# Optimization experiments

Hardware: AMD Instinct MI355X
Metric: run time of the kernel (lower is better)

Reference implementation:

```python
import jax, jax.numpy as jnp
import numpy as np

NB, H, C, HID, EMB = 4, 12, 1024, 768, 512
E, M, L, SPAN = 22, 4, 16, 32
TD, INTER = 20, 256
NN = E + E * M + L
NREL, NLAYERS = 3, 4

def _build_adj():
    # static relational adjacency: r0 entity<->its mentions, r1 mention<->co-entity mention, r2 mention<->link
    A = np.zeros((NREL, NN, NN), np.float32)
    for e in range(E):
        for m in range(M):
            mi = E + e * M + m
            A[0, e, mi] = A[0, mi, e] = 1.0
            for m2 in range(M):
                if m2 != m:
                    A[1, mi, E + e * M + m2] = 1.0
            li = E + E * M + ((e * M + m) % L)
            A[2, mi, li] = A[2, li, mi] = 1.0
    A = A / (A.sum(-1, keepdims=True) + 1e-5)
    return jnp.asarray(A)

_ADJ = _build_adj()
_TYPES = np.concatenate([np.zeros(E, np.int32), np.ones(E * M, np.int32), np.full(L, 2, np.int32)])

def _forward(sequence_output, attention, W_trans, b_trans, type_embed,
             rgcn_Wrel0, rgcn_Wself0, rgcn_Wrel, rgcn_Wself,
             fs_w1, fs_b1, fs_g1, fs_be1, fs_w2, fs_b2, fs_g2, fs_be2,
             fc_w1, fc_b1, fc_g1, fc_be1, fc_w2, fc_b2, fc_g2, fc_be2,
             cr_w1, cr_b1, cr_w2, cr_b2, cr_w3, cr_b3,
             mention_idx, link_start):
    n = sequence_output.shape[0]
    b = jnp.arange(n)[:, None, None]
    seq = sequence_output @ W_trans + b_trans            # [n,C,EMB] extractor_trans
    attq = attention.transpose(0, 2, 1, 3)               # [n,C,H,C] query-major
    # --- make_graph: mention / entity nodes (gather + logsumexp pooling) ---
    m_rep = seq[b, mention_idx]                          # [n,E,M,EMB]
    m_att = attq[b, mention_idx]                         # [n,E,M,H,C]
    e_rep = jax.nn.logsumexp(m_rep, axis=2)              # [n,E,EMB]
    e_att = m_att.mean(axis=2)                           # [n,E,H,C]
    # --- link nodes: attention-weighted span pooling ---
    idx = link_start[:, :, None] + jnp.arange(SPAN)      # [n,L,SPAN]
    span = seq[b, idx]                                   # [n,L,SPAN,EMB]
    att_rows = attq[b, idx]                              # [n,L,SPAN,H,C]
    col_idx = jnp.broadcast_to(idx[:, :, None, None, :], (n, L, SPAN, H, SPAN))
    block = jnp.take_along_axis(att_rows, col_idx, axis=4).mean(axis=3)  # [n,L,SPAN,SPAN]
    link_rep = jnp.einsum('nlst,nltd->nld', block, span) / SPAN          # [n,L,EMB]
    # --- node matrix + type embedding ---
    nodes = jnp.concatenate([e_rep, m_rep.reshape(n, E * M, EMB), link_rep], axis=1)
    tfeat = jnp.broadcast_to(type_embed[_TYPES][None], (n, NN, TD))
    h = jnp.concatenate([nodes, tfeat], axis=-1)         # [n,NN,EMB+TD]
    # --- RGCN ---
    def rgcn_layer(hh, Wrel, Wself):
        msg = jnp.einsum('rij,njd,rdo->nio', _ADJ, hh, Wrel)
        return jax.nn.relu(msg + hh @ Wself)
    h = rgcn_layer(h, rgcn_Wrel0, rgcn_Wself0)
    for l in range(NLAYERS - 1):
        h = rgcn_layer(h, rgcn_Wrel[l], rgcn_Wself[l])
    # --- relation_map: structure + attention-weighted context ---
    entity_stru = h[:, :E]                               # [n,E,EMB]
    ea = e_att.mean(axis=2)                              # [n,E,C]
    ea = ea / (ea.sum(-1, keepdims=True) + 1e-5)
    e_ctx = jnp.einsum('nec,ncd->ned', ea, seq)          # [n,E,EMB]
    ec = entity_stru + e_ctx
    fmap = (ec[:, :, None, :] * ec[:, None, :, :]).transpose(0, 3, 1, 2)  # [n,EMB,E,E]
    # --- SE fusion (fusion_s / fusion_c, BN in eval form) ---
    conv1x1 = lambda x, w, bb: jnp.einsum('nchw,oc->nohw', x, w) + bb[None, :, None, None]
    bn = lambda x, g, be: x * g[None, :, None, None] + be[None, :, None, None]
    s = bn(conv1x1(jax.nn.relu(bn(conv1x1(fmap, fs_w1, fs_b1), fs_g1, fs_be1)), fs_w2, fs_b2), fs_g2, fs_be2)
    pooled = fmap.mean(axis=(2, 3), keepdims=True)
    cb = bn(conv1x1(jax.nn.relu(bn(conv1x1(pooled, fc_w1, fc_b1), fc_g1, fc_be1)), fc_w2, fc_b2), fc_g2, fc_be2)
    fused = fmap * jax.nn.sigmoid(s + cb)
    # --- conv_reason 5x5 blocks ---
    dn = ('NCHW', 'OIHW', 'NCHW')
    conv = lambda x, w, bb: jax.lax.conv_general_dilated(x, w, (1, 1), 'SAME', dimension_numbers=dn) + bb[None, :, None, None]
    r = jax.nn.relu(conv(fused, cr_w1, cr_b1))
    r = jax.nn.relu(conv(r, cr_w2, cr_b2))
    return jax.nn.relu(conv(r, cr_w3, cr_b3))            # [n,EMB,E,E]

def setup_inputs():
    key = jax.random.key(0)
    ks = jax.random.split(key, 24)
    p = lambda k, sh: jax.random.normal(k, sh, jnp.float32) * 0.02
    z = lambda sh: jnp.zeros(sh, jnp.float32)
    o = lambda sh: jnp.ones(sh, jnp.float32)
    return {
        'sequence_output': jax.random.normal(ks[0], (NB, C, HID), jnp.float32),
        'attention': jax.random.uniform(ks[1], (NB, H, C, C), jnp.float32),
        'W_trans': p(ks[2], (HID, EMB)), 'b_trans': z((EMB,)),
        'type_embed': p(ks[3], (3, TD)),
        'rgcn_Wrel0': p(ks[4], (NREL, EMB + TD, EMB)), 'rgcn_Wself0': p(ks[5], (EMB + TD, EMB)),
        'rgcn_Wrel': p(ks[6], (NLAYERS - 1, NREL, EMB, EMB)), 'rgcn_Wself': p(ks[7], (NLAYERS - 1, EMB, EMB)),
        'fs_w1': p(ks[8], (INTER, EMB)), 'fs_b1': z((INTER,)), 'fs_g1': o((INTER,)), 'fs_be1': z((INTER,)),
        'fs_w2': p(ks[9], (EMB, INTER)), 'fs_b2': z((EMB,)), 'fs_g2': o((EMB,)), 'fs_be2': z((EMB,)),
        'fc_w1': p(ks[10], (INTER, EMB)), 'fc_b1': z((INTER,)), 'fc_g1': o((INTER,)), 'fc_be1': z((INTER,)),
        'fc_w2': p(ks[11], (EMB, INTER)), 'fc_b2': z((EMB,)), 'fc_g2': o((EMB,)), 'fc_be2': z((EMB,)),
        'cr_w1': p(ks[12], (INTER, EMB, 5, 5)), 'cr_b1': z((INTER,)),
        'cr_w2': p(ks[13], (INTER, INTER, 5, 5)), 'cr_b2': z((INTER,)),
        'cr_w3': p(ks[14], (EMB, INTER, 5, 5)), 'cr_b3': z((EMB,)),
        'mention_idx': jax.random.randint(ks[15], (NB, E, M), 0, C),
        'link_start': jnp.sort(jax.random.randint(ks[16], (NB, L), 0, C - SPAN), axis=-1),
    }

def reference(sequence_output, attention, W_trans, b_trans, type_embed,
              rgcn_Wrel0, rgcn_Wself0, rgcn_Wrel, rgcn_Wself,
              fs_w1, fs_b1, fs_g1, fs_be1, fs_w2, fs_b2, fs_g2, fs_be2,
              fc_w1, fc_b1, fc_g1, fc_be1, fc_w2, fc_b2, fc_g2, fc_be2,
              cr_w1, cr_b1, cr_w2, cr_b2, cr_w3, cr_b3,
              mention_idx, link_start):
    return _forward(sequence_output, attention, W_trans, b_trans, type_embed,
                    rgcn_Wrel0, rgcn_Wself0, rgcn_Wrel, rgcn_Wself,
                    fs_w1, fs_b1, fs_g1, fs_be1, fs_w2, fs_b2, fs_g2, fs_be2,
                    fc_w1, fc_b1, fc_g1, fc_be1, fc_w2, fc_b2, fc_g2, fc_be2,
                    cr_w1, cr_b1, cr_w2, cr_b2, cr_w3, cr_b3,
                    mention_idx, link_start)
```

## Files before the change

kernel.cpp:

```cpp
#include <hip/hip_runtime.h>
#include <hip/hip_bf16.h>
#include <stdint.h>

typedef long long ll;
typedef float f32x4 __attribute__((ext_vector_type(4)));
typedef __bf16 bf16x8 __attribute__((ext_vector_type(8)));
typedef __bf16 bf16x4 __attribute__((ext_vector_type(4)));

__global__ void k_prep(const float* __restrict__ cr_w1, const float* __restrict__ cr_w2,
                       const float* __restrict__ cr_w3, __bf16* __restrict__ Wt1,
                       __bf16* __restrict__ Wt2, __bf16* __restrict__ Wt3,
                       const float* __restrict__ W_trans, __bf16* __restrict__ wth,
                       __bf16* __restrict__ wtl,
                       const float* __restrict__ Wrel0, const float* __restrict__ Wself0,
                       __bf16* __restrict__ wc0h, __bf16* __restrict__ wc0l,
                       const float* __restrict__ Wrel, const float* __restrict__ Wself,
                       __bf16* __restrict__ wc13h, __bf16* __restrict__ wc13l)
{
  __shared__ float t[32][33];
  int b = blockIdx.x; int tid = threadIdx.x;
  if (b < 1024){
    const float* w; __bf16* dst; int C, o;
    if (b < 256){ w=cr_w1; dst=Wt1; C=512; o=b; }
    else if (b < 512){ w=cr_w2; dst=Wt2; C=256; o=b-256; }
    else { w=cr_w3; dst=Wt3; C=256; o=b-512; }
    for (int c=tid; c<C; c+=256){
      const float* src = w + ((size_t)o*C + c)*25;
      float v[25];
      #pragma unroll
      for (int q=0;q<25;q++) v[q] = src[q];
      #pragma unroll
      for (int q=0;q<25;q++) dst[((size_t)o*25 + q)*C + c] = (__bf16)v[q];
    }
  } else if (b < 2560){
    ll idx = (ll)(b-1024)*256 + tid;
    int r = (int)(idx % 768); int c = (int)(idx / 768);
    float x = W_trans[(ll)r*512 + c];
    __bf16 h = (__bf16)x;
    wth[idx] = h; wtl[idx] = (__bf16)(x - (float)h);
  } else {
    int Din, Kpad, bx, by;
    const float* wr; const float* ws2; __bf16* hb; __bf16* lb;
    if (b < 3648){
      int b2 = b-2560; bx = b2 % 68; by = b2/68; Din=532; Kpad=2176;
      wr = Wrel0; ws2 = Wself0; hb = wc0h; lb = wc0l;
    } else {
      int b3 = b-3648; int l = b3/1024; int r2 = b3%1024; bx = r2%64; by = r2/64;
      Din=512; Kpad=2048;
      wr = Wrel + (ll)l*3*512*512; ws2 = Wself + (ll)l*512*512;
      hb = wc13h + (ll)l*512*2048; lb = wc13l + (ll)l*512*2048;
    }
    int k0 = bx*32, o0 = by*32;
    int tx = tid&31, ty = tid>>5;
    for (int j=ty; j<32; j+=8){
      int k = k0 + j; float v = 0.f;
      if (k < 3*Din) v = wr[(ll)k*512 + o0+tx];
      else if (k < 4*Din) v = ws2[(ll)(k-3*Din)*512 + o0+tx];
      t[j][tx] = v;
    }
    __syncthreads();
    for (int j=ty; j<32; j+=8){
      float x = t[tx][j];
      __bf16 h = (__bf16)x;
      hb[(ll)(o0+j)*Kpad + k0+tx] = h;
      lb[(ll)(o0+j)*Kpad + k0+tx] = (__bf16)(x - (float)h);
    }
  }
}

template<int SPLIT, int MODE, int BN>
__global__ __launch_bounds__(512) void gemm_mfma(
    const float* __restrict__ A,
    const __bf16* __restrict__ Bhi, const __bf16* __restrict__ Blo,
    float* __restrict__ Cf, __bf16* __restrict__ Cb,
    int M, int N, int K, ll sA, ll sB, ll sC,
    const float* __restrict__ biasN, const float* __restrict__ biasM,
    const float* __restrict__ gM, const float* __restrict__ beM,
    const __bf16* __restrict__ Fm, const float* __restrict__ CBV)
{
  constexpr int NF = BN/32;
  constexpr int SL = (4096 + BN*64) * (SPLIT?2:1);
  constexpr int REDB = 256*2*NF*16;
  constexpr int LDSB = (2*SL > REDB) ? 2*SL : REDB;
  __shared__ char lds[LDSB];

  int b = blockIdx.z;
  A += sA*b; Bhi += sB*b; if (SPLIT) Blo += sB*b;

  const int tid = threadIdx.x;
  const int slice = tid>>8;
  const int tl = tid & 255;
  const int w4 = (tid>>6)&3;
  const int grp = tid>>8;
  const int l15 = tid&15, lg=(tid&63)>>4, lg16=lg*16;
  const int wave_m0=(w4>>1)*32, wave_n0=(w4&1)*(BN/2);
  const int m0 = blockIdx.y*64, n0 = blockIdx.x*BN;

  char* sA_H = lds + slice*SL;
  char* sB_H = sA_H + 4096;
  char* sA_L = sB_H + BN*64;
  char* sB_L = sA_L + 4096;

  const int sa_row=tl>>2, sa_c8=tl&3;
  const int sa_byte = sa_row*64 + ((sa_c8*16) ^ (((sa_row>>1)&3)<<4));
  const int gmA = m0 + sa_row;

  int baseA[2], baseB[NF];
  #pragma unroll
  for (int mf=0; mf<2; ++mf){
    int r = wave_m0 + mf*16 + l15;
    baseA[mf] = r*64 + (lg16 ^ (((r>>1)&3)<<4));
  }
  #pragma unroll
  for (int nf=0; nf<NF; ++nf){
    int r = wave_n0 + nf*16 + l15;
    baseB[nf] = r*64 + (lg16 ^ (((r>>1)&3)<<4));
  }

  f32x4 acc[2][NF] = {};

  for (int k0=0; k0<K; k0+=64){
    int kk = k0 + slice*32;
    __syncthreads();
    {
      float f[8] = {0,0,0,0,0,0,0,0};
      if (gmA < M){
        float4 p0 = *reinterpret_cast<const float4*>(A + (ll)gmA*K + kk + sa_c8*8);
        float4 p1 = *reinterpret_cast<const float4*>(A + (ll)gmA*K + kk + sa_c8*8 + 4);
        f[0]=p0.x; f[1]=p0.y; f[2]=p0.z; f[3]=p0.w;
        f[4]=p1.x; f[5]=p1.y; f[6]=p1.z; f[7]=p1.w;
      }
      bf16x8 h, l;
      #pragma unroll
      for (int j=0;j<8;j++){
        h[j] = (__bf16)f[j];
        if (SPLIT) l[j] = (__bf16)(f[j] - (float)h[j]);
      }
      *reinterpret_cast<bf16x8*>(sA_H + sa_byte) = h;
      if (SPLIT) *reinterpret_cast<bf16x8*>(sA_L + sa_byte) = l;
    }
    #pragma unroll
    for (int i=0;i<BN/64;i++){
      int idx = tl + i*256;
      int row = idx>>2, c8 = idx&3;
      int gn = n0 + row;
      int byte = row*64 + ((c8*16) ^ (((row>>1)&3)<<4));
      bf16x8 v = {};
      if (gn < N) v = *reinterpret_cast<const bf16x8*>(Bhi + (ll)gn*K + kk + c8*8);
      *reinterpret_cast<bf16x8*>(sB_H + byte) = v;
      if (SPLIT){
        bf16x8 vl = {};
        if (gn < N) vl = *reinterpret_cast<const bf16x8*>(Blo + (ll)gn*K + kk + c8*8);
        *reinterpret_cast<bf16x8*>(sB_L + byte) = vl;
      }
    }
    __syncthreads();
    bf16x8 aH[2], bH[NF];
    #pragma unroll
    for (int mf=0; mf<2; ++mf) aH[mf] = *reinterpret_cast<const bf16x8*>(sA_H + baseA[mf]);
    #pragma unroll
    for (int nf=0; nf<NF; ++nf) bH[nf] = *reinterpret_cast<const bf16x8*>(sB_H + baseB[nf]);
    if (SPLIT){
      bf16x8 aL[2], bL[NF];
      #pragma unroll
      for (int mf=0; mf<2; ++mf) aL[mf] = *reinterpret_cast<const bf16x8*>(sA_L + baseA[mf]);
      #pragma unroll
      for (int nf=0; nf<NF; ++nf) bL[nf] = *reinterpret_cast<const bf16x8*>(sB_L + baseB[nf]);
      #pragma unroll
      for (int mf=0; mf<2; ++mf)
        #pragma unroll
        for (int nf=0; nf<NF; ++nf){
          acc[mf][nf] = __builtin_amdgcn_mfma_f32_16x16x32_bf16(aH[mf], bH[nf], acc[mf][nf], 0,0,0);
          acc[mf][nf] = __builtin_amdgcn_mfma_f32_16x16x32_bf16(aH[mf], bL[nf], acc[mf][nf], 0,0,0);
          acc[mf][nf] = __builtin_amdgcn_mfma_f32_16x16x32_bf16(aL[mf], bH[nf], acc[mf][nf], 0,0,0);
        }
    } else {
      #pragma unroll
      for (int mf=0; mf<2; ++mf)
        #pragma unroll
        for (int nf=0; nf<NF; ++nf)
          acc[mf][nf] = __builtin_amdgcn_mfma_f32_16x16x32_bf16(aH[mf], bH[nf], acc[mf][nf], 0,0,0);
    }
  }

  __syncthreads();
  if (grp==1){
    char* rp = lds + (ll)(tid-256)*(2*NF*16);
    #pragma unroll
    for (int mf=0; mf<2; ++mf)
      #pragma unroll
      for (int nf=0; nf<NF; ++nf)
        *reinterpret_cast<f32x4*>(rp + (mf*NF+nf)*16) = acc[mf][nf];
  }
  __syncthreads();
  if (grp!=0) return;
  {
    char* rp = lds + (ll)tid*(2*NF*16);
    #pragma unroll
    for (int mf=0; mf<2; ++mf)
      #pragma unroll
      for (int nf=0; nf<NF; ++nf)
        acc[mf][nf] += *reinterpret_cast<f32x4*>(rp + (mf*NF+nf)*16);
  }

  if (MODE==0 || MODE==1){
    float* C = Cf + sC*b;
    #pragma unroll
    for (int mf=0; mf<2; ++mf){
      int gmb = m0 + wave_m0 + mf*16 + lg*4;
      #pragma unroll
      for (int nf=0; nf<NF; ++nf){
        int gn = n0 + wave_n0 + nf*16 + l15;
        if (gn >= N) continue;
        float bn_ = (MODE==0 && biasN) ? biasN[gn] : 0.f;
        f32x4 a = acc[mf][nf];
        #pragma unroll
        for (int r=0;r<4;r++){
          int gm = gmb + r;
          if (gm < M){
            float v = a[r] + bn_;
            if (MODE==1) v = fmaxf(v, 0.f);
            C[(ll)gm*N + gn] = v;
          }
        }
      }
    }
  } else if (MODE==2){
    __bf16* C = Cb + sC*b;
    #pragma unroll
    for (int mf=0; mf<2; ++mf){
      int gmb = m0 + wave_m0 + mf*16 + lg*4;
      float b0=biasM[gmb], b1=biasM[gmb+1], b2=biasM[gmb+2], b3=biasM[gmb+3];
      float g0=gM[gmb], g1=gM[gmb+1], g2=gM[gmb+2], g3=gM[gmb+3];
      float e0=beM[gmb], e1=beM[gmb+1], e2=beM[gmb+2], e3=beM[gmb+3];
      #pragma unroll
      for (int nf=0; nf<NF; ++nf){
        int gn = n0 + wave_n0 + nf*16 + l15;
        if (gn >= N) continue;
        f32x4 a = acc[mf][nf];
        union { bf16x4 v; uint2 u; } pk;
        pk.v[0] = (__bf16)fmaxf((a[0]+b0)*g0+e0, 0.f);
        pk.v[1] = (__bf16)fmaxf((a[1]+b1)*g1+e1, 0.f);
        pk.v[2] = (__bf16)fmaxf((a[2]+b2)*g2+e2, 0.f);
        pk.v[3] = (__bf16)fmaxf((a[3]+b3)*g3+e3, 0.f);
        *reinterpret_cast<uint2*>(C + (ll)gn*M + gmb) = pk.u;
      }
    }
  } else {
    __bf16* C = Cb + sC*b;
    const __bf16* fm = Fm + (ll)b*484*512;
    const float* cb = CBV + (ll)b*512;
    #pragma unroll
    for (int mf=0; mf<2; ++mf){
      int gmb = m0 + wave_m0 + mf*16 + lg*4;
      float b0=biasM[gmb], b1=biasM[gmb+1], b2=biasM[gmb+2], b3=biasM[gmb+3];
      float g0=gM[gmb], g1=gM[gmb+1], g2=gM[gmb+2], g3=gM[gmb+3];
      float e0=beM[gmb], e1=beM[gmb+1], e2=beM[gmb+2], e3=beM[gmb+3];
      float c0=cb[gmb], c1=cb[gmb+1], c2=cb[gmb+2], c3=cb[gmb+3];
      #pragma unroll
      for (int nf=0; nf<NF; ++nf){
        int gn = n0 + wave_n0 + nf*16 + l15;
        if (gn >= N) continue;
        f32x4 a = acc[mf][nf];
        bf16x4 fmv = *reinterpret_cast<const bf16x4*>(fm + (ll)gn*512 + gmb);
        float s0 = (a[0]+b0)*g0+e0 + c0;
        float s1 = (a[1]+b1)*g1+e1 + c1;
        float s2 = (a[2]+b2)*g2+e2 + c2;
        float s3 = (a[3]+b3)*g3+e3 + c3;
        union { bf16x4 v; uint2 u; } pk;
        pk.v[0] = (__bf16)((float)fmv[0] / (1.f + expf(-s0)));
        pk.v[1] = (__bf16)((float)fmv[1] / (1.f + expf(-s1)));
        pk.v[2] = (__bf16)((float)fmv[2] / (1.f + expf(-s2)));
        pk.v[3] = (__bf16)((float)fmv[3] / (1.f + expf(-s3)));
        int py = gn/22, px = gn%22;
        int e = (py+2)*32 + px + 2;
        *reinterpret_cast<uint2*>(C + (ll)e*512 + gmb) = pk.u;
      }
    }
  }
}

template<int CIN, int OCHT, bool FINAL>
__global__ __launch_bounds__(256) void conv5_mfma(
    const __bf16* __restrict__ Xg, const __bf16* __restrict__ Wt,
    const float* __restrict__ bias, __bf16* __restrict__ Xout,
    float* __restrict__ outF)
{
  __shared__ bf16x8 Xs8[272*32/8];
  __shared__ bf16x8 Ws8[5*64*32/8];
  char* xs = (char*)Xs8;
  char* wsm = (char*)Ws8;

  const int tid = threadIdx.x;
  const int l = tid & 63;
  const int l15 = l & 15, lg = l >> 4, lg16 = (l>>4)*16;
  const int w = tid >> 6;
  const int wave_o0 = (w>>1)*32;
  const int wave_p0 = (w&1)*64;
  const int b = blockIdx.z;
  const int p0 = blockIdx.x*128;
  const int o0 = blockIdx.y*64;

  int orow0 = wave_o0 + l15;
  int orow1 = wave_o0 + 16 + l15;
  int baseA0 = orow0*64 + (lg16 ^ (((orow0>>1)&3)<<4));
  int baseA1 = orow1*64 + (lg16 ^ (((orow1>>1)&3)<<4));
  int pl[4];
  #pragma unroll
  for (int pf=0; pf<4; ++pf) pl[pf] = wave_p0 + pf*16 + l15;

  f32x4 acc[2][4] = {};

  const int NCB = CIN/32;
  for (int cblk=0; cblk<NCB; ++cblk){
    __syncthreads();
    #pragma unroll
    for (int i=0;i<5;i++){
      int idx = tid + i*256;
      if (idx < 1088){
        int e = idx>>2, c8 = idx&3;
        const __bf16* g = Xg + ((size_t)(b*928 + p0 + e))*CIN + cblk*32 + c8*8;
        bf16x8 v = *reinterpret_cast<const bf16x8*>(g);
        int byte = e*64 + ((c8*16) ^ (((e>>1)&3)<<4));
        *reinterpret_cast<bf16x8*>(xs + byte) = v;
      }
    }
    for (int g5=0; g5<5; ++g5){
      if (g5>0) __syncthreads();
      #pragma unroll
      for (int i=0;i<5;i++){
        int idx = tid + i*256;
        int tapL = idx>>8, r = idx&255;
        int o = r>>2, c8 = r&3;
        const __bf16* g = Wt + ((size_t)(o0+o)*25 + (g5*5+tapL))*CIN + cblk*32 + c8*8;
        bf16x8 v = *reinterpret_cast<const bf16x8*>(g);
        int byte = tapL*4096 + o*64 + ((c8*16) ^ (((o>>1)&3)<<4));
        *reinterpret_cast<bf16x8*>(wsm + byte) = v;
      }
      __syncthreads();
      #pragma unroll
      for (int tapL=0; tapL<5; ++tapL){
        bf16x8 a0 = *reinterpret_cast<const bf16x8*>(wsm + tapL*4096 + baseA0);
        bf16x8 a1 = *reinterpret_cast<const bf16x8*>(wsm + tapL*4096 + baseA1);
        int koff = g5*32 + tapL;
        #pragma unroll
        for (int pf=0; pf<4; ++pf){
          int e = pl[pf] + koff;
          bf16x8 bv = *reinterpret_cast<const bf16x8*>(xs + e*64 + (lg16 ^ (((e>>1)&3)<<4)));
          acc[0][pf] = __builtin_amdgcn_mfma_f32_16x16x32_bf16(a0, bv, acc[0][pf], 0,0,0);
          acc[1][pf] = __builtin_amdgcn_mfma_f32_16x16x32_bf16(a1, bv, acc[1][pf], 0,0,0);
        }
      }
    }
  }

  #pragma unroll
  for (int of=0; of<2; ++of){
    int og = o0 + wave_o0 + of*16 + lg*4;
    float b0 = bias[og], b1 = bias[og+1], b2 = bias[og+2], b3 = bias[og+3];
    #pragma unroll
    for (int pf=0; pf<4; ++pf){
      int p = p0 + pl[pf];
      int py = p>>5, px = p&31;
      if (py>=22 || px>=22) continue;
      f32x4 a = acc[of][pf];
      float v0 = fmaxf(a[0]+b0, 0.f), v1 = fmaxf(a[1]+b1, 0.f);
      float v2 = fmaxf(a[2]+b2, 0.f), v3 = fmaxf(a[3]+b3, 0.f);
      if (FINAL){
        size_t base = ((size_t)b*OCHT + og)*484 + py*22 + px;
        outF[base] = v0; outF[base+484] = v1; outF[base+968] = v2; outF[base+1452] = v3;
      } else {
        union { bf16x4 v; uint2 u; } pk;
        pk.v[0] = (__bf16)v0; pk.v[1] = (__bf16)v1; pk.v[2] = (__bf16)v2; pk.v[3] = (__bf16)v3;
        int e = p + 66;
        *reinterpret_cast<uint2*>(Xout + ((size_t)(b*928 + e))*OCHT + og) = pk.u;
      }
    }
  }
}

__global__ void k_gather(const float* __restrict__ seq, const float* __restrict__ att,
                         const int* __restrict__ midx, const int* __restrict__ ls_,
                         const float* __restrict__ te, float* __restrict__ h0,
                         float* __restrict__ ea, __bf16* __restrict__ sqTh,
                         __bf16* __restrict__ sqTl)
{
  __shared__ float part[32][8];
  __shared__ float wv[32];
  __shared__ float vals[1024];
  __shared__ float red[256];
  __shared__ float tt2[32][33];
  int b = blockIdx.x; int t = threadIdx.x;
  if (b < 88){
    int n = b/22, e = b%22;
    int rows[4];
    #pragma unroll
    for (int m=0;m<4;m++) rows[m] = midx[(n*22+e)*4+m];
    for (int d=t; d<512; d+=256){
      float v[4]; float mx = -1e30f;
      #pragma unroll
      for (int m=0;m<4;m++){
        v[m] = seq[((ll)n*1024+rows[m])*512 + d];
        h0[((ll)n*126+22+e*4+m)*532 + d] = v[m];
        mx = fmaxf(mx, v[m]);
      }
      float s = 0.f;
      #pragma unroll
      for (int m=0;m<4;m++) s += expf(v[m]-mx);
      h0[((ll)n*126+e)*532 + d] = mx + logf(s);
    }
  } else if (b < 152){
    int bb = b-88;
    int n = bb/16, l = bb%16;
    int ls = ls_[n*16+l];
    int tt = t>>3, lane = t&7;
    float acc = 0.f;
    for (int i=lane; i<384; i+=8){
      int h = i>>5, s = i&31;
      acc += att[((ll)(n*12+h)*1024 + ls+s)*1024 + (ls+tt)];
    }
    part[tt][lane] = acc; __syncthreads();
    if (lane==0){
      float s2=0.f;
      #pragma unroll
      for (int q=0;q<8;q++) s2 += part[tt][q];
      wv[tt] = s2*(1.f/12.f);
    }
    __syncthreads();
    for (int d=t; d<512; d+=256){
      float a2 = 0.f;
      for (int tk=0;tk<32;tk++) a2 += wv[tk]*seq[((ll)n*1024+ls+tk)*512 + d];
      h0[((ll)n*126+110+l)*532 + d] = a2*(1.f/32.f);
    }
  } else if (b < 192){
    int idx = (b-152)*256 + t;
    if (idx < 4*126*20){
      int q = idx%20; int i = (idx/20)%126; int n = idx/(20*126);
      int ty = (i<22)?0:((i<110)?1:2);
      h0[((ll)n*126+i)*532 + 512 + q] = te[ty*20+q];
    }
  } else if (b < 280){
    int bb = b-192;
    int n = bb/22, e = bb%22;
    int rows[4];
    #pragma unroll
    for (int m=0;m<4;m++) rows[m] = midx[(n*22+e)*4+m];
    float local = 0.f;
    for (int c=t; c<1024; c+=256){
      float acc = 0.f;
      #pragma unroll
      for (int m=0;m<4;m++){
        const float* base = att + ((ll)n*12*1024 + rows[m])*1024 + c;
        #pragma unroll
        for (int h=0;h<12;h++) acc += base[(ll)h*1048576];
      }
      acc *= (1.f/48.f);
      vals[c] = acc; local += acc;
    }
    red[t] = local; __syncthreads();
    for (int s=128;s>0;s>>=1){ if (t<s) red[t]+=red[t+s]; __syncthreads(); }
    float denom = red[0] + 1e-5f;
    for (int c=t; c<1024; c+=256) ea[((ll)bb)*1024 + c] = vals[c]/denom;
  } else {
    int b2 = b-280;
    int n = b2>>9; int rem = b2&511;
    int r0 = (rem&31)*32, c0 = (rem>>5)*32;
    int tx = t&31, ty = t>>5;
    for (int j=ty; j<32; j+=8)
      tt2[j][tx] = seq[((ll)n*1024 + r0+j)*512 + c0+tx];
    __syncthreads();
    for (int j=ty; j<32; j+=8){
      float x = tt2[tx][j];
      __bf16 h = (__bf16)x;
      ll o = ((ll)n*512 + c0+j)*1024 + r0+tx;
      sqTh[o] = h; sqTl[o] = (__bf16)(x - (float)h);
    }
  }
}

__global__ void k_buildX_s(const float* __restrict__ h, float* __restrict__ X,
                           int Din, int ldX){
  int n = blockIdx.x/126, i = blockIdx.x%126;
  const float* hb = h + (ll)n*126*Din;
  ll rowoff = (ll)(n*126+i)*ldX;
  const float inv1 = 1.f/(1.f+1e-5f), inv3 = 1.f/(3.f+1e-5f), inv4 = 1.f/(4.f+1e-5f);
  for (int d=threadIdx.x; d<Din; d+=256){
    float m0v=0.f, m1v=0.f, m2v=0.f;
    if (i < 22){
      int base = 22 + i*4;
      float s = hb[(ll)(base+0)*Din+d] + hb[(ll)(base+1)*Din+d]
              + hb[(ll)(base+2)*Din+d] + hb[(ll)(base+3)*Din+d];
      m0v = s * inv4;
    } else if (i < 110){
      int em = i-22, e = em>>2, base = 22+(e<<2);
      m0v = hb[(ll)e*Din+d] * inv1;
      float s1 = 0.f;
      #pragma unroll
      for (int m2=0;m2<4;m2++) if (base+m2 != i) s1 += hb[(ll)(base+m2)*Din+d];
      m1v = s1 * inv3;
      m2v = hb[(ll)(110+(em&15))*Din+d] * inv1;
    } else {
      int li0 = i-110;
      int cnt = (li0<8)?6:5;
      float s = 0.f;
      for (int t2=0;t2<cnt;t2++) s += hb[(ll)(22+li0+16*t2)*Din+d];
      m2v = s / ((float)cnt + 1e-5f);
    }
    float hh = hb[(ll)i*Din+d];
    X[rowoff + 0*Din + d] = m0v;
    X[rowoff + 1*Din + d] = m1v;
    X[rowoff + 2*Din + d] = m2v;
    X[rowoff + 3*Din + d] = hh;
  }
  for (int k=4*Din+threadIdx.x; k<ldX; k+=256) X[rowoff + k] = 0.f;
}

__global__ void k_fmap2(const float* __restrict__ hfin, const float* __restrict__ ectx,
                        __bf16* __restrict__ fmapT,
                        const float* __restrict__ w1, const float* __restrict__ b1,
                        const float* __restrict__ g1, const float* __restrict__ be1,
                        const float* __restrict__ w2, const float* __restrict__ b2,
                        const float* __restrict__ g2, const float* __restrict__ be2,
                        float* __restrict__ cb){
  __shared__ float ps[512], t1[256];
  int b = blockIdx.x; int t = threadIdx.x;
  if (b < 3872){
    int idx = b*256 + t;
    int ch = idx & 511; int p = (idx>>9) % 484; int n = idx/(484*512);
    int i = p/22, j = p%22;
    float vi = hfin[((ll)n*126+i)*512 + ch] + ectx[((ll)n*22+i)*512 + ch];
    float vj = hfin[((ll)n*126+j)*512 + ch] + ectx[((ll)n*22+j)*512 + ch];
    fmapT[idx] = (__bf16)(vi*vj);
  } else {
    int n = b-3872;
    for (int c=t; c<512; c+=256){
      float s = 0.f;
      for (int i=0;i<22;i++)
        s += hfin[((ll)n*126+i)*512 + c] + ectx[((ll)n*22+i)*512 + c];
      ps[c] = s*s*(1.f/484.f);
    }
    __syncthreads();
    {
      float acc = 0.f;
      for (int c=0;c<512;c++) acc += w1[t*512+c]*ps[c];
      float v = g1[t]*(acc+b1[t]) + be1[t];
      t1[t] = fmaxf(v, 0.f);
    }
    __syncthreads();
    for (int o=t; o<512; o+=256){
      float acc = 0.f;
      for (int c=0;c<256;c++) acc += w2[o*256+c]*t1[c];
      cb[n*512+o] = g2[o]*(acc+b2[o]) + be2[o];
    }
  }
}

extern "C" void kernel_launch(void* const* d_in, const int* in_sizes, int n_in,
                              void* d_out, int out_size, void* d_ws, size_t ws_size,
                              hipStream_t stream)
{
  (void)in_sizes; (void)n_in; (void)out_size; (void)ws_size;
  const float* seqout   = (const float*)d_in[0];
  const float* att      = (const float*)d_in[1];
  const float* W_trans  = (const float*)d_in[2];
  const float* b_trans  = (const float*)d_in[3];
  const float* type_emb = (const float*)d_in[4];
  const float* Wrel0    = (const float*)d_in[5];
  const float* Wself0   = (const float*)d_in[6];
  const float* Wrel     = (const float*)d_in[7];
  const float* Wself    = (const float*)d_in[8];
  const float* fs_w1    = (const float*)d_in[9];
  const float* fs_b1    = (const float*)d_in[10];
  const float* fs_g1    = (const float*)d_in[11];
  const float* fs_be1   = (const float*)d_in[12];
  const float* fs_w2    = (const float*)d_in[13];
  const float* fs_b2    = (const float*)d_in[14];
  const float* fs_g2    = (const float*)d_in[15];
  const float* fs_be2   = (const float*)d_in[16];
  const float* fc_w1    = (const float*)d_in[17];
  const float* fc_b1    = (const float*)d_in[18];
  const float* fc_g1    = (const float*)d_in[19];
  const float* fc_be1   = (const float*)d_in[20];
  const float* fc_w2    = (const float*)d_in[21];
  const float* fc_b2    = (const float*)d_in[22];
  const float* fc_g2    = (const float*)d_in[23];
  const float* fc_be2   = (const float*)d_in[24];
  const float* cr_w1    = (const float*)d_in[25];
  const float* cr_b1    = (const float*)d_in[26];
  const float* cr_w2    = (const float*)d_in[27];
  const float* cr_b2    = (const float*)d_in[28];
  const float* cr_w3    = (const float*)d_in[29];
  const float* cr_b3    = (const float*)d_in[30];
  const int*   midx     = (const int*)d_in[31];
  const int*   lstart   = (const int*)d_in[32];
  float* out            = (float*)d_out;

  char* wsb = (char*)d_ws;
  size_t off = 0;
  auto allocB = [&](size_t nbytes)->char*{ char* p = wsb + off; off += (nbytes + 63) & ~(size_t)63; return p; };
  float* seq   = (float*)allocB((size_t)4096*512*4);
  float* h0    = (float*)allocB((size_t)504*532*4);
  float* ea    = (float*)allocB((size_t)88*1024*4);
  float* ectx  = (float*)allocB((size_t)88*512*4);
  float* X     = (float*)allocB((size_t)504*2176*4);
  float* hA    = (float*)allocB((size_t)504*512*4);
  float* hB    = (float*)allocB((size_t)504*512*4);
  float* cbv   = (float*)allocB(2048*4);
  __bf16* wth  = (__bf16*)allocB((size_t)512*768*2);
  __bf16* wtl  = (__bf16*)allocB((size_t)512*768*2);
  __bf16* sqTh = (__bf16*)allocB((size_t)4*512*1024*2);
  __bf16* sqTl = (__bf16*)allocB((size_t)4*512*1024*2);
  __bf16* wc0h = (__bf16*)allocB((size_t)512*2176*2);
  __bf16* wc0l = (__bf16*)allocB((size_t)512*2176*2);
  __bf16* wc13h= (__bf16*)allocB((size_t)3*512*2048*2);
  __bf16* wc13l= (__bf16*)allocB((size_t)3*512*2048*2);
  __bf16* fmapT= (__bf16*)allocB((size_t)4*484*512*2);
  __bf16* s1bT = (__bf16*)allocB((size_t)4*484*256*2);
  __bf16* Xint1 = (__bf16*)allocB((size_t)4*928*512*2);
  __bf16* Xint2 = (__bf16*)allocB((size_t)4*928*256*2);
  __bf16* Xint3 = (__bf16*)allocB((size_t)4*928*256*2);
  __bf16* Wt1   = (__bf16*)allocB((size_t)256*25*512*2);
  __bf16* Wt2   = (__bf16*)allocB((size_t)256*25*256*2);
  __bf16* Wt3   = (__bf16*)allocB((size_t)512*25*256*2);

  (void)hipMemsetAsync(Xint1, 0, (size_t)(4*928*512 + 4*928*256 + 4*928*256)*2, stream);

  k_prep<<<6720,256,0,stream>>>(cr_w1, cr_w2, cr_w3, Wt1, Wt2, Wt3,
                                W_trans, wth, wtl,
                                Wrel0, Wself0, wc0h, wc0l,
                                Wrel, Wself, wc13h, wc13l);

  gemm_mfma<1,0,128><<<dim3(4,64,1),512,0,stream>>>(seqout, wth, wtl, seq, nullptr,
      4096,512,768, 0,0,0, b_trans,nullptr,nullptr,nullptr, nullptr,nullptr);
  k_gather<<<2328,256,0,stream>>>(seq, att, midx, lstart, type_emb, h0, ea, sqTh, sqTl);
  gemm_mfma<1,0,64><<<dim3(8,1,4),512,0,stream>>>(ea, sqTh, sqTl, ectx, nullptr,
      22,512,1024, (ll)22*1024, (ll)512*1024, (ll)22*512,
      nullptr,nullptr,nullptr,nullptr, nullptr,nullptr);
  k_buildX_s<<<504,256,0,stream>>>(h0, X, 532, 2176);
  gemm_mfma<1,1,64><<<dim3(8,8,1),512,0,stream>>>(X, wc0h, wc0l, hA, nullptr,
      504,512,2176, 0,0,0, nullptr,nullptr,nullptr,nullptr, nullptr,nullptr);
  float* hcur = hA; float* hnxt = hB;
  for (int l=0;l<3;l++){
    k_buildX_s<<<504,256,0,stream>>>(hcur, X, 512, 2048);
    gemm_mfma<1,1,64><<<dim3(8,8,1),512,0,stream>>>(X,
        wc13h + (ll)l*512*2048, wc13l + (ll)l*512*2048, hnxt, nullptr,
        504,512,2048, 0,0,0, nullptr,nullptr,nullptr,nullptr, nullptr,nullptr);
    float* t = hcur; hcur = hnxt; hnxt = t;
  }
  k_fmap2<<<3876,256,0,stream>>>(hcur, ectx, fmapT,
                                 fc_w1, fc_b1, fc_g1, fc_be1,
                                 fc_w2, fc_b2, fc_g2, fc_be2, cbv);
  gemm_mfma<0,2,64><<<dim3(8,4,4),512,0,stream>>>(fs_w1, fmapT, nullptr, nullptr, s1bT,
      256,484,512, 0, (ll)484*512, (ll)484*256,
      nullptr, fs_b1, fs_g1, fs_be1, nullptr,nullptr);
  gemm_mfma<0,4,64><<<dim3(8,8,4),512,0,stream>>>(fs_w2, s1bT, nullptr, nullptr, Xint1,
      512,484,256, 0, (ll)484*256, (ll)928*512,
      nullptr, fs_b2, fs_g2, fs_be2, fmapT, cbv);
  conv5_mfma<512,256,false><<<dim3(6,4,4),256,0,stream>>>(Xint1, Wt1, cr_b1, Xint2, nullptr);
  conv5_mfma<256,256,false><<<dim3(6,4,4),256,0,stream>>>(Xint2, Wt2, cr_b2, Xint3, nullptr);
  conv5_mfma<256,512,true ><<<dim3(6,8,4),256,0,stream>>>(Xint3, Wt3, cr_b3, nullptr, out);
}
```

Baseline: 532.9 us.

## Fuse RGCN message aggregation into GEMM A-load and compute entity context directly

Removes the k_buildX_s kernels by having the RGCN GEMM build its A tile on the fly, aggregating neighbour rows per relation from the static adjacency structure. The self and weight layout is padded per relation block (KD) so each 8-wide chunk maps to a single relation. The entity-context GEMM and the bf16 transpose of seq are replaced by a direct weighted sum inside k_gather. This cuts four launches and the X round trip through memory. In exchange the GEMM A-loads become scalar, gathered and redundant, and the per-block context loop is serial over 1024 rows.

```diff
diff --git a/kernel.cpp b/kernel.cpp
--- a/kernel.cpp
+++ b/kernel.cpp
@@ -39,14 +39,14 @@
     __bf16 h = (__bf16)x;
     wth[idx] = h; wtl[idx] = (__bf16)(x - (float)h);
   } else {
-    int Din, Kpad, bx, by;
+    int Din, Kpad, KD, bx, by;
     const float* wr; const float* ws2; __bf16* hb; __bf16* lb;
     if (b < 3648){
-      int b2 = b-2560; bx = b2 % 68; by = b2/68; Din=532; Kpad=2176;
+      int b2 = b-2560; bx = b2 % 68; by = b2/68; Din=532; Kpad=2176; KD=544;
       wr = Wrel0; ws2 = Wself0; hb = wc0h; lb = wc0l;
     } else {
       int b3 = b-3648; int l = b3/1024; int r2 = b3%1024; bx = r2%64; by = r2/64;
-      Din=512; Kpad=2048;
+      Din=512; Kpad=2048; KD=512;
       wr = Wrel + (ll)l*3*512*512; ws2 = Wself + (ll)l*512*512;
       hb = wc13h + (ll)l*512*2048; lb = wc13l + (ll)l*512*2048;
     }
@@ -54,8 +54,9 @@
     int tx = tid&31, ty = tid>>5;
     for (int j=ty; j<32; j+=8){
       int k = k0 + j; float v = 0.f;
-      if (k < 3*Din) v = wr[(ll)k*512 + o0+tx];
-      else if (k < 4*Din) v = ws2[(ll)(k-3*Din)*512 + o0+tx];
+      int r = k / KD, d = k - r*KD;
+      if (d < Din && r < 4)
+        v = (r<3) ? wr[((ll)(r*Din+d))*512 + o0+tx] : ws2[(ll)d*512 + o0+tx];
       t[j][tx] = v;
     }
     __syncthreads();
@@ -68,7 +69,7 @@
   }
 }
 
-template<int SPLIT, int MODE, int BN>
+template<int SPLIT, int MODE, int BN, int RGCN>
 __global__ __launch_bounds__(512) void gemm_mfma(
     const float* __restrict__ A,
     const __bf16* __restrict__ Bhi, const __bf16* __restrict__ Blo,
@@ -76,7 +77,8 @@
     int M, int N, int K, ll sA, ll sB, ll sC,
     const float* __restrict__ biasN, const float* __restrict__ biasM,
     const float* __restrict__ gM, const float* __restrict__ beM,
-    const __bf16* __restrict__ Fm, const float* __restrict__ CBV)
+    const __bf16* __restrict__ Fm, const float* __restrict__ CBV,
+    int Din, int KD)
 {
   constexpr int NF = BN/32;
   constexpr int SL = (4096 + BN*64) * (SPLIT?2:1);
@@ -105,6 +107,9 @@
   const int sa_byte = sa_row*64 + ((sa_c8*16) ^ (((sa_row>>1)&3)<<4));
   const int gmA = m0 + sa_row;
 
+  int rg_n = 0, rg_i = 0;
+  if (RGCN){ rg_n = gmA/126; rg_i = gmA - rg_n*126; }
+
   int baseA[2], baseB[NF];
   #pragma unroll
   for (int mf=0; mf<2; ++mf){
@@ -124,11 +129,62 @@
     __syncthreads();
     {
       float f[8] = {0,0,0,0,0,0,0,0};
-      if (gmA < M){
-        float4 p0 = *reinterpret_cast<const float4*>(A + (ll)gmA*K + kk + sa_c8*8);
-        float4 p1 = *reinterpret_cast<const float4*>(A + (ll)gmA*K + kk + sa_c8*8 + 4);
-        f[0]=p0.x; f[1]=p0.y; f[2]=p0.z; f[3]=p0.w;
-        f[4]=p1.x; f[5]=p1.y; f[6]=p1.z; f[7]=p1.w;
+      if (!RGCN){
+        if (gmA < M){
+          float4 p0 = *reinterpret_cast<const float4*>(A + (ll)gmA*K + kk + sa_c8*8);
+          float4 p1 = *reinterpret_cast<const float4*>(A + (ll)gmA*K + kk + sa_c8*8 + 4);
+          f[0]=p0.x; f[1]=p0.y; f[2]=p0.z; f[3]=p0.w;
+          f[4]=p1.x; f[5]=p1.y; f[6]=p1.z; f[7]=p1.w;
+        }
+      } else {
+        const float inv1 = 1.f/(1.f+1e-5f), inv3 = 1.f/(3.f+1e-5f), inv4 = 1.f/(4.f+1e-5f);
+        int kchunk = kk + sa_c8*8;
+        int r = kchunk / KD;
+        int d0 = kchunk - r*KD;
+        if (gmA < M){
+          const float* hb = A + (ll)rg_n*126*Din;
+          int i = rg_i;
+          if (r==3){
+            #pragma unroll
+            for (int j=0;j<8;j++){ int d=d0+j; if (d<Din) f[j]=hb[(ll)i*Din+d]; }
+          } else if (i < 22){
+            if (r==0){
+              int base = 22 + i*4;
+              #pragma unroll
+              for (int j=0;j<8;j++){ int d=d0+j; if (d<Din)
+                f[j] = (hb[(ll)(base+0)*Din+d]+hb[(ll)(base+1)*Din+d]
+                       +hb[(ll)(base+2)*Din+d]+hb[(ll)(base+3)*Din+d])*inv4; }
+            }
+          } else if (i < 110){
+            int em = i-22, e = em>>2, base = 22+(e<<2);
+            if (r==0){
+              #pragma unroll
+              for (int j=0;j<8;j++){ int d=d0+j; if (d<Din) f[j]=hb[(ll)e*Din+d]*inv1; }
+            } else if (r==1){
+              #pragma unroll
+              for (int j=0;j<8;j++){ int d=d0+j; if (d<Din){
+                float s1 = 0.f;
+                #pragma unroll
+                for (int m2=0;m2<4;m2++) if (base+m2 != i) s1 += hb[(ll)(base+m2)*Din+d];
+                f[j] = s1*inv3; } }
+            } else {
+              int li = 110 + (em&15);
+              #pragma unroll
+              for (int j=0;j<8;j++){ int d=d0+j; if (d<Din) f[j]=hb[(ll)li*Din+d]*inv1; }
+            }
+          } else {
+            if (r==2){
+              int li0 = i-110;
+              int cnt = (li0<8)?6:5;
+              float invc = 1.f/((float)cnt + 1e-5f);
+              #pragma unroll
+              for (int j=0;j<8;j++){ int d=d0+j; if (d<Din){
+                float s = 0.f;
+                for (int t2=0;t2<cnt;t2++) s += hb[(ll)(22+li0+16*t2)*Din+d];
+                f[j] = s*invc; } }
+            }
+          }
+        }
       }
       bf16x8 h, l;
       #pragma unroll
@@ -382,14 +438,12 @@
 __global__ void k_gather(const float* __restrict__ seq, const float* __restrict__ att,
                          const int* __restrict__ midx, const int* __restrict__ ls_,
                          const float* __restrict__ te, float* __restrict__ h0,
-                         float* __restrict__ ea, __bf16* __restrict__ sqTh,
-                         __bf16* __restrict__ sqTl)
+                         float* __restrict__ ectx)
 {
   __shared__ float part[32][8];
   __shared__ float wv[32];
   __shared__ float vals[1024];
   __shared__ float red[256];
-  __shared__ float tt2[32][33];
   int b = blockIdx.x; int t = threadIdx.x;
   if (b < 88){
     int n = b/22, e = b%22;
@@ -439,7 +493,7 @@
       int ty = (i<22)?0:((i<110)?1:2);
       h0[((ll)n*126+i)*532 + 512 + q] = te[ty*20+q];
     }
-  } else if (b < 280){
+  } else {
     int bb = b-192;
     int n = bb/22, e = bb%22;
     int rows[4];
@@ -459,60 +513,19 @@
     }
     red[t] = local; __syncthreads();
     for (int s=128;s>0;s>>=1){ if (t<s) red[t]+=red[t+s]; __syncthreads(); }
-    float denom = red[0] + 1e-5f;
-    for (int c=t; c<1024; c+=256) ea[((ll)bb)*1024 + c] = vals[c]/denom;
-  } else {
-    int b2 = b-280;
-    int n = b2>>9; int rem = b2&511;
-    int r0 = (rem&31)*32, c0 = (rem>>5)*32;
-    int tx = t&31, ty = t>>5;
-    for (int j=ty; j<32; j+=8)
-      tt2[j][tx] = seq[((ll)n*1024 + r0+j)*512 + c0+tx];
-    __syncthreads();
-    for (int j=ty; j<32; j+=8){
-      float x = tt2[tx][j];
-      __bf16 h = (__bf16)x;
-      ll o = ((ll)n*512 + c0+j)*1024 + r0+tx;
-      sqTh[o] = h; sqTl[o] = (__bf16)(x - (float)h);
-    }
-  }
-}
-
-__global__ void k_buildX_s(const float* __restrict__ h, float* __restrict__ X,
-                           int Din, int ldX){
-  int n = blockIdx.x/126, i = blockIdx.x%126;
-  const float* hb = h + (ll)n*126*Din;
-  ll rowoff = (ll)(n*126+i)*ldX;
-  const float inv1 = 1.f/(1.f+1e-5f), inv3 = 1.f/(3.f+1e-5f), inv4 = 1.f/(4.f+1e-5f);
-  for (int d=threadIdx.x; d<Din; d+=256){
-    float m0v=0.f, m1v=0.f, m2v=0.f;
-    if (i < 22){
-      int base = 22 + i*4;
-      float s = hb[(ll)(base+0)*Din+d] + hb[(ll)(base+1)*Din+d]
-              + hb[(ll)(base+2)*Din+d] + hb[(ll)(base+3)*Din+d];
-      m0v = s * inv4;
-    } else if (i < 110){
-      int em = i-22, e = em>>2, base = 22+(e<<2);
-      m0v = hb[(ll)e*Din+d] * inv1;
-      float s1 = 0.f;
-      #pragma unroll
-      for (int m2=0;m2<4;m2++) if (base+m2 != i) s1 += hb[(ll)(base+m2)*Din+d];
-      m1v = s1 * inv3;
-      m2v = hb[(ll)(110+(em&15))*Din+d] * inv1;
-    } else {
-      int li0 = i-110;
-      int cnt = (li0<8)?6:5;
-      float s = 0.f;
-      for (int t2=0;t2<cnt;t2++) s += hb[(ll)(22+li0+16*t2)*Din+d];
-      m2v = s / ((float)cnt + 1e-5f);
-    }
-    float hh = hb[(ll)i*Din+d];
-    X[rowoff + 0*Din + d] = m0v;
-    X[rowoff + 1*Din + d] = m1v;
-    X[rowoff + 2*Din + d] = m2v;
-    X[rowoff + 3*Din + d] = hh;
-  }
-  for (int k=4*Din+threadIdx.x; k<ldX; k+=256) X[rowoff + k] = 0.f;
+    float inv = 1.f/(red[0] + 1e-5f);
+    for (int c=t; c<1024; c+=256) vals[c] *= inv;
+    __syncthreads();
+    float a0 = 0.f, a1 = 0.f;
+    #pragma unroll 4
+    for (int c=0;c<1024;c++){
+      float v = vals[c];
+      const float* s = seq + ((ll)n*1024+c)*512;
+      a0 += v*s[t]; a1 += v*s[t+256];
+    }
+    ectx[((ll)n*22+e)*512 + t]       = a0;
+    ectx[((ll)n*22+e)*512 + t + 256] = a1;
+  }
 }
 
 __global__ void k_fmap2(const float* __restrict__ hfin, const float* __restrict__ ectx,
@@ -600,16 +613,12 @@
   auto allocB = [&](size_t nbytes)->char*{ char* p = wsb + off; off += (nbytes + 63) & ~(size_t)63; return p; };
   float* seq   = (float*)allocB((size_t)4096*512*4);
   float* h0    = (float*)allocB((size_t)504*532*4);
-  float* ea    = (float*)allocB((size_t)88*1024*4);
   float* ectx  = (float*)allocB((size_t)88*512*4);
-  float* X     = (float*)allocB((size_t)504*2176*4);
   float* hA    = (float*)allocB((size_t)504*512*4);
   float* hB    = (float*)allocB((size_t)504*512*4);
   float* cbv   = (float*)allocB(2048*4);
   __bf16* wth  = (__bf16*)allocB((size_t)512*768*2);
   __bf16* wtl  = (__bf16*)allocB((size_t)512*768*2);
-  __bf16* sqTh = (__bf16*)allocB((size_t)4*512*1024*2);
-  __bf16* sqTl = (__bf16*)allocB((size_t)4*512*1024*2);
   __bf16* wc0h = (__bf16*)allocB((size_t)512*2176*2);
   __bf16* wc0l = (__bf16*)allocB((size_t)512*2176*2);
   __bf16* wc13h= (__bf16*)allocB((size_t)3*512*2048*2);
@@ -630,32 +639,27 @@
                                 Wrel0, Wself0, wc0h, wc0l,
                                 Wrel, Wself, wc13h, wc13l);
 
-  gemm_mfma<1,0,128><<<dim3(4,64,1),512,0,stream>>>(seqout, wth, wtl, seq, nullptr,
-      4096,512,768, 0,0,0, b_trans,nullptr,nullptr,nullptr, nullptr,nullptr);
-  k_gather<<<2328,256,0,stream>>>(seq, att, midx, lstart, type_emb, h0, ea, sqTh, sqTl);
-  gemm_mfma<1,0,64><<<dim3(8,1,4),512,0,stream>>>(ea, sqTh, sqTl, ectx, nullptr,
-      22,512,1024, (ll)22*1024, (ll)512*1024, (ll)22*512,
-      nullptr,nullptr,nullptr,nullptr, nullptr,nullptr);
-  k_buildX_s<<<504,256,0,stream>>>(h0, X, 532, 2176);
-  gemm_mfma<1,1,64><<<dim3(8,8,1),512,0,stream>>>(X, wc0h, wc0l, hA, nullptr,
-      504,512,2176, 0,0,0, nullptr,nullptr,nullptr,nullptr, nullptr,nullptr);
+  gemm_mfma<1,0,128,0><<<dim3(4,64,1),512,0,stream>>>(seqout, wth, wtl, seq, nullptr,
+      4096,512,768, 0,0,0, b_trans,nullptr,nullptr,nullptr, nullptr,nullptr, 0,0);
+  k_gather<<<280,256,0,stream>>>(seq, att, midx, lstart, type_emb, h0, ectx);
+  gemm_mfma<1,1,64,1><<<dim3(8,8,1),512,0,stream>>>(h0, wc0h, wc0l, hA, nullptr,
+      504,512,2176, 0,0,0, nullptr,nullptr,nullptr,nullptr, nullptr,nullptr, 532,544);
   float* hcur = hA; float* hnxt = hB;
   for (int l=0;l<3;l++){
-    k_buildX_s<<<504,256,0,stream>>>(hcur, X, 512, 2048);
-    gemm_mfma<1,1,64><<<dim3(8,8,1),512,0,stream>>>(X,
+    gemm_mfma<1,1,64,1><<<dim3(8,8,1),512,0,stream>>>(hcur,
         wc13h + (ll)l*512*2048, wc13l + (ll)l*512*2048, hnxt, nullptr,
-        504,512,2048, 0,0,0, nullptr,nullptr,nullptr,nullptr, nullptr,nullptr);
+        504,512,2048, 0,0,0, nullptr,nullptr,nullptr,nullptr, nullptr,nullptr, 512,512);
     float* t = hcur; hcur = hnxt; hnxt = t;
   }
   k_fmap2<<<3876,256,0,stream>>>(hcur, ectx, fmapT,
                                  fc_w1, fc_b1, fc_g1, fc_be1,
                                  fc_w2, fc_b2, fc_g2, fc_be2, cbv);
-  gemm_mfma<0,2,64><<<dim3(8,4,4),512,0,stream>>>(fs_w1, fmapT, nullptr, nullptr, s1bT,
+  gemm_mfma<0,2,64,0><<<dim3(8,4,4),512,0,stream>>>(fs_w1, fmapT, nullptr, nullptr, s1bT,
       256,484,512, 0, (ll)484*512, (ll)484*256,
-      nullptr, fs_b1, fs_g1, fs_be1, nullptr,nullptr);
-  gemm_mfma<0,4,64><<<dim3(8,8,4),512,0,stream>>>(fs_w2, s1bT, nullptr, nullptr, Xint1,
+      nullptr, fs_b1, fs_g1, fs_be1, nullptr,nullptr, 0,0);
+  gemm_mfma<0,4,64,0><<<dim3(8,8,4),512,0,stream>>>(fs_w2, s1bT, nullptr, nullptr, Xint1,
       512,484,256, 0, (ll)484*256, (ll)928*512,
-      nullptr, fs_b2, fs_g2, fs_be2, fmapT, cbv);
+      nullptr, fs_b2, fs_g2, fs_be2, fmapT, cbv, 0,0);
   conv5_mfma<512,256,false><<<dim3(6,4,4),256,0,stream>>>(Xint1, Wt1, cr_b1, Xint2, nullptr);
   conv5_mfma<256,256,false><<<dim3(6,4,4),256,0,stream>>>(Xint2, Wt2, cr_b2, Xint3, nullptr);
   conv5_mfma<256,512,true ><<<dim3(6,8,4),256,0,stream>>>(Xint3, Wt3, cr_b3, nullptr, out);
```

After: 894.2 us. 1.68x slower.

## Fuse entity-context matmul into gather kernel and pad RGCN segments per relation

Applied to the files above, without the earlier changes.

The entity attention context is now computed directly inside k_gather: normalised attention weights are multiplied against seq in fp32, replacing the seq transpose/bf16 hi-lo split and a separate batched GEMM launch. The RGCN input matrix is re-laid out so each relation segment is padded to a fixed width, and the weight-prep transpose is updated to match. This removes a launch and large transposed intermediate buffers. In exchange, 88 blocks each run a serial 1024-step reduction, which may be less parallel than the MFMA GEMM.

```diff
diff --git a/kernel.cpp b/kernel.cpp
--- a/kernel.cpp
+++ b/kernel.cpp
@@ -39,14 +39,14 @@
     __bf16 h = (__bf16)x;
     wth[idx] = h; wtl[idx] = (__bf16)(x - (float)h);
   } else {
-    int Din, Kpad, bx, by;
+    int Din, Kpad, KD, bx, by;
     const float* wr; const float* ws2; __bf16* hb; __bf16* lb;
     if (b < 3648){
-      int b2 = b-2560; bx = b2 % 68; by = b2/68; Din=532; Kpad=2176;
+      int b2 = b-2560; bx = b2 % 68; by = b2/68; Din=532; Kpad=2176; KD=544;
       wr = Wrel0; ws2 = Wself0; hb = wc0h; lb = wc0l;
     } else {
       int b3 = b-3648; int l = b3/1024; int r2 = b3%1024; bx = r2%64; by = r2/64;
-      Din=512; Kpad=2048;
+      Din=512; Kpad=2048; KD=512;
       wr = Wrel + (ll)l*3*512*512; ws2 = Wself + (ll)l*512*512;
       hb = wc13h + (ll)l*512*2048; lb = wc13l + (ll)l*512*2048;
     }
@@ -54,8 +54,9 @@
     int tx = tid&31, ty = tid>>5;
     for (int j=ty; j<32; j+=8){
       int k = k0 + j; float v = 0.f;
-      if (k < 3*Din) v = wr[(ll)k*512 + o0+tx];
-      else if (k < 4*Din) v = ws2[(ll)(k-3*Din)*512 + o0+tx];
+      int r = k / KD, d = k - r*KD;
+      if (d < Din && r < 4)
+        v = (r<3) ? wr[((ll)(r*Din+d))*512 + o0+tx] : ws2[(ll)d*512 + o0+tx];
       t[j][tx] = v;
     }
     __syncthreads();
@@ -382,14 +383,12 @@
 __global__ void k_gather(const float* __restrict__ seq, const float* __restrict__ att,
                          const int* __restrict__ midx, const int* __restrict__ ls_,
                          const float* __restrict__ te, float* __restrict__ h0,
-                         float* __restrict__ ea, __bf16* __restrict__ sqTh,
-                         __bf16* __restrict__ sqTl)
+                         float* __restrict__ ectx)
 {
   __shared__ float part[32][8];
   __shared__ float wv[32];
   __shared__ float vals[1024];
   __shared__ float red[256];
-  __shared__ float tt2[32][33];
   int b = blockIdx.x; int t = threadIdx.x;
   if (b < 88){
     int n = b/22, e = b%22;
@@ -439,7 +438,7 @@
       int ty = (i<22)?0:((i<110)?1:2);
       h0[((ll)n*126+i)*532 + 512 + q] = te[ty*20+q];
     }
-  } else if (b < 280){
+  } else {
     int bb = b-192;
     int n = bb/22, e = bb%22;
     int rows[4];
@@ -459,60 +458,57 @@
     }
     red[t] = local; __syncthreads();
     for (int s=128;s>0;s>>=1){ if (t<s) red[t]+=red[t+s]; __syncthreads(); }
-    float denom = red[0] + 1e-5f;
-    for (int c=t; c<1024; c+=256) ea[((ll)bb)*1024 + c] = vals[c]/denom;
-  } else {
-    int b2 = b-280;
-    int n = b2>>9; int rem = b2&511;
-    int r0 = (rem&31)*32, c0 = (rem>>5)*32;
-    int tx = t&31, ty = t>>5;
-    for (int j=ty; j<32; j+=8)
-      tt2[j][tx] = seq[((ll)n*1024 + r0+j)*512 + c0+tx];
-    __syncthreads();
-    for (int j=ty; j<32; j+=8){
-      float x = tt2[tx][j];
-      __bf16 h = (__bf16)x;
-      ll o = ((ll)n*512 + c0+j)*1024 + r0+tx;
-      sqTh[o] = h; sqTl[o] = (__bf16)(x - (float)h);
-    }
+    float inv = 1.f/(red[0] + 1e-5f);
+    for (int c=t; c<1024; c+=256) vals[c] *= inv;
+    __syncthreads();
+    float a0 = 0.f, a1 = 0.f;
+    #pragma unroll 4
+    for (int c=0;c<1024;c++){
+      float v = vals[c];
+      const float* s = seq + ((ll)n*1024+c)*512;
+      a0 += v*s[t]; a1 += v*s[t+256];
+    }
+    ectx[((ll)n*22+e)*512 + t]       = a0;
+    ectx[((ll)n*22+e)*512 + t + 256] = a1;
   }
 }
 
 __global__ void k_buildX_s(const float* __restrict__ h, float* __restrict__ X,
-                           int Din, int ldX){
+                           int Din, int KD){
   int n = blockIdx.x/126, i = blockIdx.x%126;
   const float* hb = h + (ll)n*126*Din;
-  ll rowoff = (ll)(n*126+i)*ldX;
+  ll rowoff = (ll)(n*126+i)*4*KD;
   const float inv1 = 1.f/(1.f+1e-5f), inv3 = 1.f/(3.f+1e-5f), inv4 = 1.f/(4.f+1e-5f);
-  for (int d=threadIdx.x; d<Din; d+=256){
-    float m0v=0.f, m1v=0.f, m2v=0.f;
-    if (i < 22){
-      int base = 22 + i*4;
-      float s = hb[(ll)(base+0)*Din+d] + hb[(ll)(base+1)*Din+d]
-              + hb[(ll)(base+2)*Din+d] + hb[(ll)(base+3)*Din+d];
-      m0v = s * inv4;
-    } else if (i < 110){
-      int em = i-22, e = em>>2, base = 22+(e<<2);
-      m0v = hb[(ll)e*Din+d] * inv1;
-      float s1 = 0.f;
-      #pragma unroll
-      for (int m2=0;m2<4;m2++) if (base+m2 != i) s1 += hb[(ll)(base+m2)*Din+d];
-      m1v = s1 * inv3;
-      m2v = hb[(ll)(110+(em&15))*Din+d] * inv1;
-    } else {
-      int li0 = i-110;
-      int cnt = (li0<8)?6:5;
-      float s = 0.f;
-      for (int t2=0;t2<cnt;t2++) s += hb[(ll)(22+li0+16*t2)*Din+d];
-      m2v = s / ((float)cnt + 1e-5f);
-    }
-    float hh = hb[(ll)i*Din+d];
-    X[rowoff + 0*Din + d] = m0v;
-    X[rowoff + 1*Din + d] = m1v;
-    X[rowoff + 2*Din + d] = m2v;
-    X[rowoff + 3*Din + d] = hh;
-  }
-  for (int k=4*Din+threadIdx.x; k<ldX; k+=256) X[rowoff + k] = 0.f;
+  for (int d=threadIdx.x; d<KD; d+=256){
+    float m0v=0.f, m1v=0.f, m2v=0.f, hh=0.f;
+    if (d < Din){
+      if (i < 22){
+        int base = 22 + i*4;
+        float s = hb[(ll)(base+0)*Din+d] + hb[(ll)(base+1)*Din+d]
+                + hb[(ll)(base+2)*Din+d] + hb[(ll)(base+3)*Din+d];
+        m0v = s * inv4;
+      } else if (i < 110){
+        int em = i-22, e = em>>2, base = 22+(e<<2);
+        m0v = hb[(ll)e*Din+d] * inv1;
+        float s1 = 0.f;
+        #pragma unroll
+        for (int m2=0;m2<4;m2++) if (base+m2 != i) s1 += hb[(ll)(base+m2)*Din+d];
+        m1v = s1 * inv3;
+        m2v = hb[(ll)(110+(em&15))*Din+d] * inv1;
+      } else {
+        int li0 = i-110;
+        int cnt = (li0<8)?6:5;
+        float s = 0.f;
+        for (int t2=0;t2<cnt;t2++) s += hb[(ll)(22+li0+16*t2)*Din+d];
+        m2v = s / ((float)cnt + 1e-5f);
+      }
+      hh = hb[(ll)i*Din+d];
+    }
+    X[rowoff + 0*KD + d] = m0v;
+    X[rowoff + 1*KD + d] = m1v;
+    X[rowoff + 2*KD + d] = m2v;
+    X[rowoff + 3*KD + d] = hh;
+  }
 }
 
 __global__ void k_fmap2(const float* __restrict__ hfin, const float* __restrict__ ectx,
@@ -600,7 +596,6 @@
   auto allocB = [&](size_t nbytes)->char*{ char* p = wsb + off; off += (nbytes + 63) & ~(size_t)63; return p; };
   float* seq   = (float*)allocB((size_t)4096*512*4);
   float* h0    = (float*)allocB((size_t)504*532*4);
-  float* ea    = (float*)allocB((size_t)88*1024*4);
   float* ectx  = (float*)allocB((size_t)88*512*4);
   float* X     = (float*)allocB((size_t)504*2176*4);
   float* hA    = (float*)allocB((size_t)504*512*4);
@@ -608,8 +603,6 @@
   float* cbv   = (float*)allocB(2048*4);
   __bf16* wth  = (__bf16*)allocB((size_t)512*768*2);
   __bf16* wtl  = (__bf16*)allocB((size_t)512*768*2);
-  __bf16* sqTh = (__bf16*)allocB((size_t)4*512*1024*2);
-  __bf16* sqTl = (__bf16*)allocB((size_t)4*512*1024*2);
   __bf16* wc0h = (__bf16*)allocB((size_t)512*2176*2);
   __bf16* wc0l = (__bf16*)allocB((size_t)512*2176*2);
   __bf16* wc13h= (__bf16*)allocB((size_t)3*512*2048*2);
@@ -632,16 +625,13 @@
 
   gemm_mfma<1,0,128><<<dim3(4,64,1),512,0,stream>>>(seqout, wth, wtl, seq, nullptr,
       4096,512,768, 0,0,0, b_trans,nullptr,nullptr,nullptr, nullptr,nullptr);
-  k_gather<<<2328,256,0,stream>>>(seq, att, midx, lstart, type_emb, h0, ea, sqTh, sqTl);
-  gemm_mfma<1,0,64><<<dim3(8,1,4),512,0,stream>>>(ea, sqTh, sqTl, ectx, nullptr,
-      22,512,1024, (ll)22*1024, (ll)512*1024, (ll)22*512,
-      nullptr,nullptr,nullptr,nullptr, nullptr,nullptr);
-  k_buildX_s<<<504,256,0,stream>>>(h0, X, 532, 2176);
+  k_gather<<<280,256,0,stream>>>(seq, att, midx, lstart, type_emb, h0, ectx);
+  k_buildX_s<<<504,256,0,stream>>>(h0, X, 532, 544);
   gemm_mfma<1,1,64><<<dim3(8,8,1),512,0,stream>>>(X, wc0h, wc0l, hA, nullptr,
       504,512,2176, 0,0,0, nullptr,nullptr,nullptr,nullptr, nullptr,nullptr);
   float* hcur = hA; float* hnxt = hB;
   for (int l=0;l<3;l++){
-    k_buildX_s<<<504,256,0,stream>>>(hcur, X, 512, 2048);
+    k_buildX_s<<<504,256,0,stream>>>(hcur, X, 512, 512);
     gemm_mfma<1,1,64><<<dim3(8,8,1),512,0,stream>>>(X,
         wc13h + (ll)l*512*2048, wc13l + (ll)l*512*2048, hnxt, nullptr,
         504,512,2048, 0,0,0, nullptr,nullptr,nullptr,nullptr, nullptr,nullptr);
```

After: 567.9 us. +6.6%, slower.
